# Optimization experiments

Measured on AMD Instinct MI355X. Metric: run time of the kernel, lower is better.

The kernel has to match this reference:

```python
import jax, jax.numpy as jnp
import numpy as np

WEIGHT = 0.1
N_BINS = 64
EPS = 1e-08  # fp32: max(base_eps, 1e-8)


def setup_inputs() -> dict:
    key = jax.random.key(0)
    k1, k2 = jax.random.split(key)
    pred = jax.random.normal(k1, (16, 1, 512, 512), dtype=jnp.float32)
    target = jax.random.normal(k2, (16, 1, 512, 512), dtype=jnp.float32)
    return {"pred": pred, "target": target}


def _soft_hist(x_norm, bin_centers, bin_width):
    # x_norm: [B, N]; bin_centers: [n_bins]
    # Gaussian kernel density -> sum over N -> [B, n_bins]
    diff = x_norm[:, :, None] - bin_centers[None, None, :]  # [B, N, n_bins]
    kern = jnp.exp(-(diff ** 2) / (2.0 * bin_width ** 2))
    return kern.sum(axis=1)


def reference(pred, target):
    B = pred.shape[0]
    pred_flat = pred.reshape(B, -1)
    target_flat = target.reshape(B, -1)

    vmin = target_flat.min(axis=-1, keepdims=True)
    vmax = target_flat.max(axis=-1, keepdims=True)

    bin_edges = jnp.linspace(0.0, 1.0, N_BINS + 1, dtype=pred.dtype)
    bin_centers = (bin_edges[:-1] + bin_edges[1:]) / 2
    bin_width = bin_edges[1] - bin_edges[0]

    denom = vmax - vmin + EPS
    pred_norm = (pred_flat - vmin) / denom
    target_norm = (target_flat - vmin) / denom

    pred_hist = _soft_hist(pred_norm, bin_centers, bin_width)      # [B, n_bins]
    target_hist = _soft_hist(target_norm, bin_centers, bin_width)  # [B, n_bins]

    pred_prob = pred_hist / (pred_hist.sum(axis=-1, keepdims=True) + EPS)
    target_prob = target_hist / (target_hist.sum(axis=-1, keepdims=True) + EPS)

    kl = target_prob * (jnp.log(target_prob + EPS) - jnp.log(pred_prob + EPS))
    return WEIGHT * kl.sum(axis=-1).mean()
```

## Files before the change

### kernel.cpp

```cpp
#include <hip/hip_runtime.h>
#include <math.h>

#define NB    16
#define NPB   (512*512)
#define NBINS 64
#define MMB   64
#define CB    64
#define EPSF  1e-8f
#define QF    0.84932180517f
#define L2E   1.44269504089f
#define LN2   0.69314718056f
#define RCLMP 1e30f


__global__ __launch_bounds__(256) void minmax_k(const float4* __restrict__ tgt,
                                                float* __restrict__ mmn,
                                                float* __restrict__ mmx,
                                                float* __restrict__ hist) {
    const int batch = blockIdx.x / MMB, sub = blockIdx.x % MMB;
    if (sub == 0 && threadIdx.x < 128) {
        const int tens = threadIdx.x >> 6, lane = threadIdx.x & 63;
        hist[(tens * NB + batch) * NBINS + lane] = 0.0f;
    }

    const int F4 = NPB / 4 / MMB;
    const float4* p = tgt + (size_t)batch * (NPB / 4) + (size_t)sub * F4;
    float mn = 3.4e38f, mx = -3.4e38f;
    #pragma unroll
    for (int i = 0; i < F4 / 256; ++i) {
        float4 v = p[i * 256 + threadIdx.x];
        mn = fminf(mn, fminf(fminf(v.x, v.y), fminf(v.z, v.w)));
        mx = fmaxf(mx, fmaxf(fmaxf(v.x, v.y), fmaxf(v.z, v.w)));
    }
    #pragma unroll
    for (int o = 1; o < 64; o <<= 1) {
        mn = fminf(mn, __shfl_xor(mn, o));
        mx = fmaxf(mx, __shfl_xor(mx, o));
    }
    __shared__ float smn[4], smx[4];
    const int wave = threadIdx.x >> 6, lane = threadIdx.x & 63;
    if (lane == 0) { smn[wave] = mn; smx[wave] = mx; }
    __syncthreads();
    if (threadIdx.x == 0) {
        mmn[blockIdx.x] = fminf(fminf(smn[0], smn[1]), fminf(smn[2], smn[3]));
        mmx[blockIdx.x] = fmaxf(fmaxf(smx[0], smx[1]), fmaxf(smx[2], smx[3]));
    }
}

__global__ __launch_bounds__(256, 8) void hist_k(const float4* __restrict__ pred,
                                                 const float4* __restrict__ tgt,
                                                 const float* __restrict__ mmn,
                                                 const float* __restrict__ mmx,
                                                 float* __restrict__ hist) {
    const int blk   = blockIdx.x;
    const int tens  = blk & 1;
    const int batch = (blk >> 1) & (NB - 1);
    const int chunk = blk >> 5;
    const int wave  = threadIdx.x >> 6, lane = threadIdx.x & 63;
    const int kbase = 16 * wave;

    const int F4C = NPB / 4 / CB;
    const float4* __restrict__ src = (tens ? tgt : pred)
        + (size_t)batch * (NPB / 4) + (size_t)chunk * F4C;

    float4 v = src[lane];

    float vmin = mmn[batch * MMB + lane];
    float vmax = mmx[batch * MMB + lane];
    #pragma unroll
    for (int o = 1; o < 64; o <<= 1) {
        vmin = fminf(vmin, __shfl_xor(vmin, o));
        vmax = fmaxf(vmax, __shfl_xor(vmax, o));
    }
    const float s64 = 64.0f / (vmax - vmin + EPSF);
    const float bk8 = fmaf(-vmin, s64, -0.5f) - (float)(kbase + 8);

    float acc[16];
    #pragma unroll
    for (int k = 0; k < 16; ++k) acc[k] = 0.0f;

    const float C1 = 0.60653065971f,   C2 = 0.13533528324f,
                C3 = 0.01110899654f,   C4 = 3.35462627903e-4f,
                C5 = 3.72665317208e-6f, C6 = 1.52299797447e-8f,
                C7 = 2.28973484833e-11f, C8 = 1.26641655490e-14f;

    const int NIT = F4C / 64;
    #pragma unroll 1
    for (int it = 0; it < NIT; ++it) {
        float4 vn = src[(it < NIT - 1 ? (it + 1) * 64 : 0) + lane];
        #pragma unroll
        for (int pq = 0; pq < 4; ++pq) {
            float xin = (pq == 0) ? v.x : (pq == 1) ? v.y : (pq == 2) ? v.z : v.w;
            float d  = fmaf(xin, s64, bk8);
            float x  = d * L2E;
            float r  = fminf(__builtin_amdgcn_exp2f(x),  RCLMP);
            float ri = fminf(__builtin_amdgcn_exp2f(-x), RCLMP);
            float t  = d * QF;
            float A  = __builtin_amdgcn_exp2f(-(t * t));
            float T = A;
            acc[8] += A;
            T *= r;  acc[9]  = fmaf(T, C1, acc[9]);
            T *= r;  acc[10] = fmaf(T, C2, acc[10]);
            T *= r;  acc[11] = fmaf(T, C3, acc[11]);
            T *= r;  acc[12] = fmaf(T, C4, acc[12]);
            T *= r;  acc[13] = fmaf(T, C5, acc[13]);
            T *= r;  acc[14] = fmaf(T, C6, acc[14]);
            T *= r;  acc[15] = fmaf(T, C7, acc[15]);
            float U = A;
            U *= ri; acc[7] = fmaf(U, C1, acc[7]);
            U *= ri; acc[6] = fmaf(U, C2, acc[6]);
            U *= ri; acc[5] = fmaf(U, C3, acc[5]);
            U *= ri; acc[4] = fmaf(U, C4, acc[4]);
            U *= ri; acc[3] = fmaf(U, C5, acc[3]);
            U *= ri; acc[2] = fmaf(U, C6, acc[2]);
            U *= ri; acc[1] = fmaf(U, C7, acc[1]);
            U *= ri; acc[0] = fmaf(U, C8, acc[0]);
        }
        v = vn;
    }

    float keep = 0.0f;
    #pragma unroll
    for (int i = 0; i < 16; ++i) {
        float t = acc[i];
        #pragma unroll
        for (int o = 1; o < 64; o <<= 1) t += __shfl_xor(t, o);
        if (lane == i) keep = t;
    }
    if (lane < 16)
        unsafeAtomicAdd(&hist[(tens * NB + batch) * NBINS + kbase + lane], keep);
}

__global__ __launch_bounds__(256) void final_k(const float* __restrict__ hist,
                                               float* __restrict__ out) {
    const int lane = threadIdx.x & 63, wave = threadIdx.x >> 6;
    __shared__ float wacc[4];
    float a = 0.0f;
    for (int b = wave; b < NB; b += 4) {
        float hp = hist[b * NBINS + lane];
        float ht = hist[(NB + b) * NBINS + lane];
        float sp = hp, st = ht;
        #pragma unroll
        for (int o = 1; o < 64; o <<= 1) {
            sp += __shfl_xor(sp, o);
            st += __shfl_xor(st, o);
        }
        float pp = hp / (sp + EPSF);
        float pt = ht / (st + EPSF);
        float term = pt * ((__builtin_amdgcn_logf(pt + EPSF)
                          - __builtin_amdgcn_logf(pp + EPSF)) * LN2);
        #pragma unroll
        for (int o = 1; o < 64; o <<= 1) term += __shfl_xor(term, o);
        a += term;
    }
    if (lane == 0) wacc[wave] = a;
    __syncthreads();
    if (threadIdx.x == 0)
        out[0] = 0.1f * (wacc[0] + wacc[1] + wacc[2] + wacc[3]) / (float)NB;
}

extern "C" void kernel_launch(void* const* d_in, const int* in_sizes, int n_in,
                              void* d_out, int out_size, void* d_ws, size_t ws_size,
                              hipStream_t stream) {
    const float* pred = (const float*)d_in[0];
    const float* tgt  = (const float*)d_in[1];
    float* mmn  = (float*)d_ws;
    float* mmx  = mmn + NB * MMB;
    float* hist = mmx + NB * MMB;
    float* out  = (float*)d_out;

    minmax_k<<<NB * MMB, 256, 0, stream>>>((const float4*)tgt, mmn, mmx, hist);
    hist_k  <<<2 * NB * CB, 256, 0, stream>>>((const float4*)pred, (const float4*)tgt,
                                              mmn, mmx, hist);
    final_k <<<1, 256, 0, stream>>>(hist, out);
}
```

Baseline: 115.4 us.

## Cover 32 bins per wave, reusing exponentials across two 16-bin windows

Each wave now accumulates 32 histogram bins instead of 16, and the block's four waves split into two pairs, each pair handling half of the chunk's points. The exp2 ratio terms r and ri are shared between the two 16-bin windows by rescaling them with the constants K16 and K16I, so the second window needs only one extra Gaussian exp per point. This roughly halves the transcendental work per point-bin. In exchange it doubles the accumulator registers, which is why the occupancy hint is lowered to 4 blocks. The clamp on the ratio terms is replaced by a med3 clamp on the offset d, which changes the numerical behaviour for points far from the bins.

Result: no change. 113.2 us (median of 2 runs) (-1.9%).

```diff
diff --git a/kernel.cpp b/kernel.cpp
--- a/kernel.cpp
+++ b/kernel.cpp
@@ -10,7 +10,8 @@
 #define QF    0.84932180517f
 #define L2E   1.44269504089f
 #define LN2   0.69314718056f
-#define RCLMP 1e30f
+#define K16   1.12535175e-7f
+#define K16I  8886110.5f
 
 
 __global__ __launch_bounds__(256) void minmax_k(const float4* __restrict__ tgt,
@@ -47,7 +48,60 @@
     }
 }
 
-__global__ __launch_bounds__(256, 8) void hist_k(const float4* __restrict__ pred,
+__device__ __forceinline__ void point32(float xin, float s64, float bk8,
+                                        float* __restrict__ acc) {
+    const float C1 = 0.60653065971f,    C2 = 0.13533528324f,
+                C3 = 0.01110899654f,    C4 = 3.35462627903e-4f,
+                C5 = 3.72665317208e-6f, C6 = 1.52299797447e-8f,
+                C7 = 2.28973484833e-11f, C8 = 1.26641655490e-14f;
+    float d   = fmaf(xin, s64, bk8);
+    float dc  = __builtin_amdgcn_fmed3f(d, -30.0f, 46.0f);
+    float x   = dc * L2E;
+    float r   = __builtin_amdgcn_exp2f(x);
+    float ri  = __builtin_amdgcn_exp2f(-x);
+    float t1  = dc * QF;
+    float A1  = __builtin_amdgcn_exp2f(-(t1 * t1));
+    float t2  = fmaf(dc, QF, -16.0f * QF);
+    float A2  = __builtin_amdgcn_exp2f(-(t2 * t2));
+    float r2  = r * K16;
+    float ri2 = ri * K16I;
+    float T = A1, U = A1;
+    acc[8] += A1;
+    T *= r;  acc[9]  = fmaf(T, C1, acc[9]);
+    T *= r;  acc[10] = fmaf(T, C2, acc[10]);
+    T *= r;  acc[11] = fmaf(T, C3, acc[11]);
+    T *= r;  acc[12] = fmaf(T, C4, acc[12]);
+    T *= r;  acc[13] = fmaf(T, C5, acc[13]);
+    T *= r;  acc[14] = fmaf(T, C6, acc[14]);
+    T *= r;  acc[15] = fmaf(T, C7, acc[15]);
+    U *= ri; acc[7]  = fmaf(U, C1, acc[7]);
+    U *= ri; acc[6]  = fmaf(U, C2, acc[6]);
+    U *= ri; acc[5]  = fmaf(U, C3, acc[5]);
+    U *= ri; acc[4]  = fmaf(U, C4, acc[4]);
+    U *= ri; acc[3]  = fmaf(U, C5, acc[3]);
+    U *= ri; acc[2]  = fmaf(U, C6, acc[2]);
+    U *= ri; acc[1]  = fmaf(U, C7, acc[1]);
+    U *= ri; acc[0]  = fmaf(U, C8, acc[0]);
+    float S = A2, V = A2;
+    acc[24] += A2;
+    S *= r2;  acc[25] = fmaf(S, C1, acc[25]);
+    S *= r2;  acc[26] = fmaf(S, C2, acc[26]);
+    S *= r2;  acc[27] = fmaf(S, C3, acc[27]);
+    S *= r2;  acc[28] = fmaf(S, C4, acc[28]);
+    S *= r2;  acc[29] = fmaf(S, C5, acc[29]);
+    S *= r2;  acc[30] = fmaf(S, C6, acc[30]);
+    S *= r2;  acc[31] = fmaf(S, C7, acc[31]);
+    V *= ri2; acc[23] = fmaf(V, C1, acc[23]);
+    V *= ri2; acc[22] = fmaf(V, C2, acc[22]);
+    V *= ri2; acc[21] = fmaf(V, C3, acc[21]);
+    V *= ri2; acc[20] = fmaf(V, C4, acc[20]);
+    V *= ri2; acc[19] = fmaf(V, C5, acc[19]);
+    V *= ri2; acc[18] = fmaf(V, C6, acc[18]);
+    V *= ri2; acc[17] = fmaf(V, C7, acc[17]);
+    V *= ri2; acc[16] = fmaf(V, C8, acc[16]);
+}
+
+__global__ __launch_bounds__(256, 4) void hist_k(const float4* __restrict__ pred,
                                                  const float4* __restrict__ tgt,
                                                  const float* __restrict__ mmn,
                                                  const float* __restrict__ mmx,
@@ -57,11 +111,13 @@
     const int batch = (blk >> 1) & (NB - 1);
     const int chunk = blk >> 5;
     const int wave  = threadIdx.x >> 6, lane = threadIdx.x & 63;
-    const int kbase = 16 * wave;
+    const int kwb   = 32 * (wave & 1);
+    const int pair  = wave >> 1;
 
     const int F4C = NPB / 4 / CB;
+    const int F4H = F4C / 2;
     const float4* __restrict__ src = (tens ? tgt : pred)
-        + (size_t)batch * (NPB / 4) + (size_t)chunk * F4C;
+        + (size_t)batch * (NPB / 4) + (size_t)chunk * F4C + (size_t)pair * F4H;
 
     float4 v = src[lane];
 
@@ -73,62 +129,33 @@
         vmax = fmaxf(vmax, __shfl_xor(vmax, o));
     }
     const float s64 = 64.0f / (vmax - vmin + EPSF);
-    const float bk8 = fmaf(-vmin, s64, -0.5f) - (float)(kbase + 8);
-
-    float acc[16];
-    #pragma unroll
-    for (int k = 0; k < 16; ++k) acc[k] = 0.0f;
-
-    const float C1 = 0.60653065971f,   C2 = 0.13533528324f,
-                C3 = 0.01110899654f,   C4 = 3.35462627903e-4f,
-                C5 = 3.72665317208e-6f, C6 = 1.52299797447e-8f,
-                C7 = 2.28973484833e-11f, C8 = 1.26641655490e-14f;
-
-    const int NIT = F4C / 64;
+    const float bk8 = fmaf(-vmin, s64, -0.5f) - (float)(kwb + 8);
+
+    float acc[32];
+    #pragma unroll
+    for (int k = 0; k < 32; ++k) acc[k] = 0.0f;
+
+    const int NIT = F4H / 64;
     #pragma unroll 1
     for (int it = 0; it < NIT; ++it) {
         float4 vn = src[(it < NIT - 1 ? (it + 1) * 64 : 0) + lane];
-        #pragma unroll
-        for (int pq = 0; pq < 4; ++pq) {
-            float xin = (pq == 0) ? v.x : (pq == 1) ? v.y : (pq == 2) ? v.z : v.w;
-            float d  = fmaf(xin, s64, bk8);
-            float x  = d * L2E;
-            float r  = fminf(__builtin_amdgcn_exp2f(x),  RCLMP);
-            float ri = fminf(__builtin_amdgcn_exp2f(-x), RCLMP);
-            float t  = d * QF;
-            float A  = __builtin_amdgcn_exp2f(-(t * t));
-            float T = A;
-            acc[8] += A;
-            T *= r;  acc[9]  = fmaf(T, C1, acc[9]);
-            T *= r;  acc[10] = fmaf(T, C2, acc[10]);
-            T *= r;  acc[11] = fmaf(T, C3, acc[11]);
-            T *= r;  acc[12] = fmaf(T, C4, acc[12]);
-            T *= r;  acc[13] = fmaf(T, C5, acc[13]);
-            T *= r;  acc[14] = fmaf(T, C6, acc[14]);
-            T *= r;  acc[15] = fmaf(T, C7, acc[15]);
-            float U = A;
-            U *= ri; acc[7] = fmaf(U, C1, acc[7]);
-            U *= ri; acc[6] = fmaf(U, C2, acc[6]);
-            U *= ri; acc[5] = fmaf(U, C3, acc[5]);
-            U *= ri; acc[4] = fmaf(U, C4, acc[4]);
-            U *= ri; acc[3] = fmaf(U, C5, acc[3]);
-            U *= ri; acc[2] = fmaf(U, C6, acc[2]);
-            U *= ri; acc[1] = fmaf(U, C7, acc[1]);
-            U *= ri; acc[0] = fmaf(U, C8, acc[0]);
-        }
+        point32(v.x, s64, bk8, acc);
+        point32(v.y, s64, bk8, acc);
+        point32(v.z, s64, bk8, acc);
+        point32(v.w, s64, bk8, acc);
         v = vn;
     }
 
     float keep = 0.0f;
     #pragma unroll
-    for (int i = 0; i < 16; ++i) {
+    for (int i = 0; i < 32; ++i) {
         float t = acc[i];
         #pragma unroll
         for (int o = 1; o < 64; o <<= 1) t += __shfl_xor(t, o);
         if (lane == i) keep = t;
     }
-    if (lane < 16)
-        unsafeAtomicAdd(&hist[(tens * NB + batch) * NBINS + kbase + lane], keep);
+    if (lane < 32)
+        unsafeAtomicAdd(&hist[(tens * NB + batch) * NBINS + kwb + lane], keep);
 }
 
 __global__ __launch_bounds__(256) void final_k(const float* __restrict__ hist,
```
